# Kernel tuning notes

Measured on AMD Instinct MI355X. Metric: run time of the kernel, lower is better.

The kernel has to match this reference:

```python
import jax, jax.numpy as jnp
import numpy as np

N_NODES = 100000
N_EDGES = 1600000
IN_CH = 64
HEADS = 8
OUT_CH = 16
NEG_SLOPE = 0.2  # PyG GATConv default


def setup_inputs() -> dict:
    key = jax.random.key(0)
    ks = jax.random.split(key, 6)
    x = jax.random.normal(ks[0], (N_NODES, IN_CH), dtype=jnp.float32)
    edge_index = jax.random.randint(ks[1], (2, N_EDGES), 0, N_NODES, dtype=jnp.int32)
    # learned parameters (PyG GATConv: shared lin for src/dst, att vectors, bias for concat output)
    W = jax.random.normal(ks[2], (HEADS * OUT_CH, IN_CH), dtype=jnp.float32) / np.sqrt(IN_CH)
    att_src = jax.random.normal(ks[3], (HEADS, OUT_CH), dtype=jnp.float32) / np.sqrt(OUT_CH)
    att_dst = jax.random.normal(ks[4], (HEADS, OUT_CH), dtype=jnp.float32) / np.sqrt(OUT_CH)
    bias = jax.random.normal(ks[5], (HEADS * OUT_CH,), dtype=jnp.float32) * 0.01
    return {"x": x, "edge_index": edge_index, "W": W,
            "att_src": att_src, "att_dst": att_dst, "bias": bias}


def reference(x, edge_index, W, att_src, att_dst, bias):
    n = x.shape[0]
    # linear projection -> [N, H, C]
    h = (x @ W.T).reshape(n, HEADS, OUT_CH)
    # per-node halves of the attention logit
    a_src = jnp.einsum('nhc,hc->nh', h, att_src)  # [N, H]
    a_dst = jnp.einsum('nhc,hc->nh', h, att_dst)  # [N, H]
    # add self loops (PyG default add_self_loops=True)
    loops = jnp.arange(n, dtype=edge_index.dtype)
    src = jnp.concatenate([edge_index[0], loops])
    dst = jnp.concatenate([edge_index[1], loops])
    # edge attention: leaky_relu then segment-softmax over incoming edges of dst
    e = jax.nn.leaky_relu(a_src[src] + a_dst[dst], NEG_SLOPE)  # [E+N, H]
    e_max = jax.ops.segment_max(e, dst, num_segments=n)
    e = jnp.exp(e - e_max[dst])
    denom = jax.ops.segment_sum(e, dst, num_segments=n)
    alpha = e / (denom[dst] + 1e-16)  # [E+N, H]
    # weighted scatter-add aggregation
    msg = h[src] * alpha[:, :, None]  # [E+N, H, C]
    out = jax.ops.segment_sum(msg, dst, num_segments=n).reshape(n, HEADS * OUT_CH)
    out = out + bias
    # unlinear: act='relu', norm=None
    return jax.nn.relu(out)
```

## Files before the change

kernel.cpp:

```cpp
#include <hip/hip_runtime.h>

#define N_NODESC 100000
#define N_EDGESC 1600000
#define HCC 128
#define E_TOTC (N_EDGESC + N_NODESC)
#define SCAN_NB 391
#define PROJ_NB 782
#define POS_NB 6641
#define WU_NB 36

#define FLAG_AGG 0x40000000u
#define FLAG_PRE 0x80000000u
#define VAL_MASK 0x3fffffffu

__device__ __forceinline__ float lrelu(float v) { return fmaxf(v, 0.2f * v); }
__device__ __forceinline__ unsigned short f2bf(float f) {
    unsigned u = __float_as_uint(f);
    unsigned r = ((u >> 16) & 1u) + 0x7fffu;
    return (unsigned short)((u + r) >> 16);
}

__global__ void wu_pos_kernel(const float* __restrict__ W,
                              const float* __restrict__ att_src, const float* __restrict__ att_dst,
                              float* __restrict__ WT, float* __restrict__ us_g,
                              const int* __restrict__ ei, int* __restrict__ deg,
                              int* __restrict__ posb) {
    if (blockIdx.x < WU_NB) {
        int t = blockIdx.x * 256 + threadIdx.x;
        if (t < 8192) {
            int k = t >> 7, c = t & 127;
            WT[t] = W[c * 64 + k];
        } else if (t < 9216) {
            int o = t - 8192;
            int k = o >> 4, c = o & 15;
            const int h = (c < 8) ? c : c - 8;
            const float* av = (c < 8) ? att_src : att_dst;
            float s = 0.f;
#pragma unroll
            for (int j = 0; j < 16; ++j) s += av[h * 16 + j] * W[(h * 16 + j) * 64 + k];
            us_g[o] = s;
        }
        return;
    }
    int e = (blockIdx.x - WU_NB) * 256 + threadIdx.x;
    if (e >= E_TOTC) return;
    int d = (e < N_EDGESC) ? ei[N_EDGESC + e] : (e - N_EDGESC);
    posb[e] = atomicAdd(&deg[d], 1);
}

__launch_bounds__(256, 2)
__global__ void proj_kernel(const float* __restrict__ x, const float* __restrict__ WT,
                            const float* __restrict__ us_g,
                            unsigned short* __restrict__ h16,
                            float* __restrict__ a_src, float* __restrict__ a_dst) {
    __shared__ float xs[128][68];
    __shared__ float ws[64][132];
    __shared__ float us[64][16];
    const int t = threadIdx.x;
    const int row0 = blockIdx.x * 128;

    const float4* wt4 = (const float4*)WT;
#pragma unroll
    for (int j = 0; j < 8; ++j) {
        int q = t + 256 * j;
        int k = q >> 5, c4 = q & 31;
        *(float4*)&ws[k][c4 * 4] = wt4[q];
    }
    ((float4*)&us[0][0])[t] = ((const float4*)us_g)[t];

#pragma unroll
    for (int j = 0; j < 8; ++j) {
        int f = (t + 256 * j) * 4;
        int r = f >> 6, k = f & 63;
        int gr = row0 + r;
        if (gr >= N_NODESC) gr = N_NODESC - 1;
        float4 v = *(const float4*)&x[(size_t)gr * 64 + k];
        *(float4*)&xs[r][k] = v;
    }
    __syncthreads();

    const int rg = t & 15;
    const int cg = t >> 4;
    float acc[8][8], acca[8];
#pragma unroll
    for (int i = 0; i < 8; ++i) {
        acca[i] = 0.f;
#pragma unroll
        for (int j = 0; j < 8; ++j) acc[i][j] = 0.f;
    }

#pragma unroll 4
    for (int k = 0; k < 64; ++k) {
        float xv[8];
#pragma unroll
        for (int i = 0; i < 8; ++i) xv[i] = xs[rg + 16 * i][k];
        float4 w0 = *(const float4*)&ws[k][4 * cg];
        float4 w1 = *(const float4*)&ws[k][64 + 4 * cg];
        float uv = us[k][cg];
#pragma unroll
        for (int i = 0; i < 8; ++i) {
            acc[i][0] += xv[i] * w0.x; acc[i][1] += xv[i] * w0.y;
            acc[i][2] += xv[i] * w0.z; acc[i][3] += xv[i] * w0.w;
            acc[i][4] += xv[i] * w1.x; acc[i][5] += xv[i] * w1.y;
            acc[i][6] += xv[i] * w1.z; acc[i][7] += xv[i] * w1.w;
            acca[i]   += xv[i] * uv;
        }
    }

#pragma unroll
    for (int i = 0; i < 8; ++i) {
        int gr = row0 + rg + 16 * i;
        if (gr < N_NODESC) {
            ushort4 p0, p1;
            p0.x = f2bf(acc[i][0]); p0.y = f2bf(acc[i][1]); p0.z = f2bf(acc[i][2]); p0.w = f2bf(acc[i][3]);
            p1.x = f2bf(acc[i][4]); p1.y = f2bf(acc[i][5]); p1.z = f2bf(acc[i][6]); p1.w = f2bf(acc[i][7]);
            *(ushort4*)&h16[(size_t)gr * HCC + 4 * cg] = p0;
            *(ushort4*)&h16[(size_t)gr * HCC + 64 + 4 * cg] = p1;
            if (cg < 8) a_src[(size_t)gr * 8 + cg] = acca[i];
            else        a_dst[(size_t)gr * 8 + cg - 8] = acca[i];
        }
    }
}

__global__ void scan_kernel(const int* __restrict__ deg, unsigned* __restrict__ state,
                            int* __restrict__ rowptr) {
    __shared__ int lds[256];
    __shared__ int s_prefix;
    const int b = blockIdx.x, t = threadIdx.x;
    const int i = b * 256 + t;
    const int v = (i < N_NODESC) ? deg[i] : 0;
    lds[t] = v;
    __syncthreads();
    for (int off = 1; off < 256; off <<= 1) {
        int u = 0;
        if (t >= off) u = lds[t - off];
        __syncthreads();
        if (t >= off) lds[t] += u;
        __syncthreads();
    }
    const int incl = lds[t];
    const int total = lds[255];
    if (t == 0) {
        if (b == 0) {
            atomicExch(&state[0], FLAG_PRE | (unsigned)total);
            s_prefix = 0;
        } else {
            atomicExch(&state[b], FLAG_AGG | (unsigned)total);
            unsigned run = 0;
            int j = b - 1;
            while (true) {
                unsigned s = atomicAdd(&state[j], 0u);
                if (s & FLAG_PRE) { run += s & VAL_MASK; break; }
                if (s & FLAG_AGG) { run += s & VAL_MASK; --j; }
            }
            atomicExch(&state[b], FLAG_PRE | ((unsigned)total + run));
            s_prefix = (int)run;
        }
    }
    __syncthreads();
    const int excl = s_prefix + incl - v;
    if (i <= N_NODESC) rowptr[i] = excl;
}

__global__ void scatter_kernel(const int* __restrict__ ei, const int* __restrict__ rowptr,
                               const int* __restrict__ posb, int* __restrict__ colsrc) {
    int e = blockIdx.x * 256 + threadIdx.x;
    if (e >= E_TOTC) return;
    int s, d;
    if (e < N_EDGESC) { s = ei[e]; d = ei[N_EDGESC + e]; }
    else              { s = d = e - N_EDGESC; }
    colsrc[rowptr[d] + posb[e]] = s;
}

__launch_bounds__(256, 8)
__global__ void agg_csr_kernel(const int* __restrict__ rowptr, const int* __restrict__ colsrc,
                               const float* __restrict__ a_src, const float* __restrict__ a_dst,
                               const unsigned* __restrict__ h32,
                               const float* __restrict__ bias, float* __restrict__ out) {
    const int t = threadIdx.x;
    const int L = t & 63;
    const int n = blockIdx.x * 4 + (t >> 6);
    const int hd = L >> 3;
    const int eL = L & 7;

    const int beg = rowptr[n], end = rowptr[n + 1];
    const float ad = a_dst[n * 8 + hd];

    float den = 0.f;
    float acc[16];
#pragma unroll
    for (int j = 0; j < 16; ++j) acc[j] = 0.f;

    int p = beg + eL;
    bool v0 = p < end;
    bool v1 = p + 8 < end;
    int sA = v0 ? colsrc[p] : 0;
    int sB = v1 ? colsrc[p + 8] : 0;
    float avA = v0 ? a_src[sA * 8 + hd] : 0.f;

    while (v0) {
        const uint4* hp = (const uint4*)(h32 + (size_t)sA * 64 + hd * 8);
        const uint4 ha = hp[0];
        const uint4 hb = hp[1];
        const bool v2 = p + 16 < end;
        const int sC = v2 ? colsrc[p + 16] : 0;
        const float avB = v1 ? a_src[sB * 8 + hd] : 0.f;

        const float pr = __expf(lrelu(avA + ad));
        den += pr;
        acc[0]  = fmaf(pr, __uint_as_float(ha.x << 16),         acc[0]);
        acc[1]  = fmaf(pr, __uint_as_float(ha.x & 0xffff0000u), acc[1]);
        acc[2]  = fmaf(pr, __uint_as_float(ha.y << 16),         acc[2]);
        acc[3]  = fmaf(pr, __uint_as_float(ha.y & 0xffff0000u), acc[3]);
        acc[4]  = fmaf(pr, __uint_as_float(ha.z << 16),         acc[4]);
        acc[5]  = fmaf(pr, __uint_as_float(ha.z & 0xffff0000u), acc[5]);
        acc[6]  = fmaf(pr, __uint_as_float(ha.w << 16),         acc[6]);
        acc[7]  = fmaf(pr, __uint_as_float(ha.w & 0xffff0000u), acc[7]);
        acc[8]  = fmaf(pr, __uint_as_float(hb.x << 16),         acc[8]);
        acc[9]  = fmaf(pr, __uint_as_float(hb.x & 0xffff0000u), acc[9]);
        acc[10] = fmaf(pr, __uint_as_float(hb.y << 16),         acc[10]);
        acc[11] = fmaf(pr, __uint_as_float(hb.y & 0xffff0000u), acc[11]);
        acc[12] = fmaf(pr, __uint_as_float(hb.z << 16),         acc[12]);
        acc[13] = fmaf(pr, __uint_as_float(hb.z & 0xffff0000u), acc[13]);
        acc[14] = fmaf(pr, __uint_as_float(hb.w << 16),         acc[14]);
        acc[15] = fmaf(pr, __uint_as_float(hb.w & 0xffff0000u), acc[15]);

        p += 8;
        sA = sB; sB = sC; avA = avB;
        v0 = v1; v1 = v2;
    }

    den += __shfl_xor(den, 1); den += __shfl_xor(den, 2); den += __shfl_xor(den, 4);
#pragma unroll
    for (int j = 0; j < 16; ++j) {
        acc[j] += __shfl_xor(acc[j], 1);
        acc[j] += __shfl_xor(acc[j], 2);
        acc[j] += __shfl_xor(acc[j], 4);
    }
    const float inv = 1.f / (den + 1e-16f);
    float ox = acc[0], oy = acc[1];
#pragma unroll
    for (int j = 1; j < 8; ++j) {
        ox = (eL == j) ? acc[2 * j]     : ox;
        oy = (eL == j) ? acc[2 * j + 1] : oy;
    }
    const float2 b = ((const float2*)bias)[L];
    float2 o;
    o.x = fmaxf(ox * inv + b.x, 0.f);
    o.y = fmaxf(oy * inv + b.y, 0.f);
    ((float2*)out)[(size_t)n * 64 + L] = o;
}

extern "C" void kernel_launch(void* const* d_in, const int* in_sizes, int n_in,
                              void* d_out, int out_size, void* d_ws, size_t ws_size,
                              hipStream_t stream) {
    const float* x       = (const float*)d_in[0];
    const int*   ei      = (const int*)d_in[1];
    const float* W       = (const float*)d_in[2];
    const float* att_src = (const float*)d_in[3];
    const float* att_dst = (const float*)d_in[4];
    const float* bias    = (const float*)d_in[5];
    float* out = (float*)d_out;

    float* ws    = (float*)d_ws;
    unsigned short* h16 = (unsigned short*)ws;
    float* a_src = ws + 6400000;
    float* a_dst = a_src + 800000;
    float* WT    = a_dst + 800000;
    float* us_g  = WT + 8192;
    int* deg     = (int*)(us_g + 1024);
    unsigned* state = (unsigned*)(deg + 100000);
    int* rowptr  = (int*)(state + 392);
    int* posb    = rowptr + 100001;
    int* colsrc  = posb + 1700000;

    hipMemsetAsync(deg, 0, (100000 + 392) * sizeof(int), stream);

    wu_pos_kernel<<<WU_NB + POS_NB, 256, 0, stream>>>(W, att_src, att_dst, WT, us_g,
                                                      ei, deg, posb);
    proj_kernel<<<PROJ_NB, 256, 0, stream>>>(x, WT, us_g, h16, a_src, a_dst);
    scan_kernel<<<SCAN_NB, 256, 0, stream>>>(deg, state, rowptr);
    scatter_kernel<<<(E_TOTC + 255) / 256, 256, 0, stream>>>(ei, rowptr, posb, colsrc);
    agg_csr_kernel<<<N_NODESC / 4, 256, 0, stream>>>(rowptr, colsrc, a_src, a_dst,
                                                     (const unsigned*)h16, bias, out);
}
```

Measured before the change: 234.9 us.

## Store features in head-major planes and split aggregation per head

The projection now writes h, a_src and a_dst in head-major planes so each head's data is contiguous. Aggregation launches eight times as many blocks, one head per block, and each lane handles two channels for one edge slot. The aim is a smaller per-head working set that stays in cache during random neighbor gathers, plus fewer registers per thread. In exchange, each edge's colsrc and rowptr is read eight times, gathers shrink to 4 bytes, and seven of every eight lanes sit idle at write-out.

```diff
diff --git a/kernel.cpp b/kernel.cpp
--- a/kernel.cpp
+++ b/kernel.cpp
@@ -51,8 +51,8 @@
 __launch_bounds__(256, 2)
 __global__ void proj_kernel(const float* __restrict__ x, const float* __restrict__ WT,
                             const float* __restrict__ us_g,
-                            unsigned short* __restrict__ h16,
-                            float* __restrict__ a_src, float* __restrict__ a_dst) {
+                            unsigned short* __restrict__ hplane,
+                            float* __restrict__ a_src_p, float* __restrict__ a_dst_p) {
     __shared__ float xs[128][68];
     __shared__ float ws[64][132];
     __shared__ float us[64][16];
@@ -107,6 +107,8 @@
         }
     }
 
+    const int hA = cg >> 2, hB = 4 + (cg >> 2);
+    const int o4 = 4 * (cg & 3);
 #pragma unroll
     for (int i = 0; i < 8; ++i) {
         int gr = row0 + rg + 16 * i;
@@ -114,10 +116,10 @@
             ushort4 p0, p1;
             p0.x = f2bf(acc[i][0]); p0.y = f2bf(acc[i][1]); p0.z = f2bf(acc[i][2]); p0.w = f2bf(acc[i][3]);
             p1.x = f2bf(acc[i][4]); p1.y = f2bf(acc[i][5]); p1.z = f2bf(acc[i][6]); p1.w = f2bf(acc[i][7]);
-            *(ushort4*)&h16[(size_t)gr * HCC + 4 * cg] = p0;
-            *(ushort4*)&h16[(size_t)gr * HCC + 64 + 4 * cg] = p1;
-            if (cg < 8) a_src[(size_t)gr * 8 + cg] = acca[i];
-            else        a_dst[(size_t)gr * 8 + cg - 8] = acca[i];
+            *(ushort4*)&hplane[((size_t)hA * N_NODESC + gr) * 16 + o4] = p0;
+            *(ushort4*)&hplane[((size_t)hB * N_NODESC + gr) * 16 + o4] = p1;
+            if (cg < 8) a_src_p[(size_t)cg * N_NODESC + gr] = acca[i];
+            else        a_dst_p[(size_t)(cg - 8) * N_NODESC + gr] = acca[i];
         }
     }
 }
@@ -173,82 +175,59 @@
 }
 
 __launch_bounds__(256, 8)
-__global__ void agg_csr_kernel(const int* __restrict__ rowptr, const int* __restrict__ colsrc,
-                               const float* __restrict__ a_src, const float* __restrict__ a_dst,
-                               const unsigned* __restrict__ h32,
-                               const float* __restrict__ bias, float* __restrict__ out) {
+__global__ void agg_head_kernel(const int* __restrict__ rowptr, const int* __restrict__ colsrc,
+                                const float* __restrict__ a_src_p, const float* __restrict__ a_dst_p,
+                                const unsigned short* __restrict__ hplane,
+                                const float* __restrict__ bias, float* __restrict__ out) {
     const int t = threadIdx.x;
     const int L = t & 63;
-    const int n = blockIdx.x * 4 + (t >> 6);
-    const int hd = L >> 3;
-    const int eL = L & 7;
+    const int head = blockIdx.x & 7;
+    const int n = (blockIdx.x >> 3) * 4 + (t >> 6);
+    const int e = L & 7;
+    const int g = L >> 3;
 
     const int beg = rowptr[n], end = rowptr[n + 1];
-    const float ad = a_dst[n * 8 + hd];
-
-    float den = 0.f;
-    float acc[16];
-#pragma unroll
-    for (int j = 0; j < 16; ++j) acc[j] = 0.f;
-
-    int p = beg + eL;
+    const float ad = a_dst_p[(size_t)head * N_NODESC + n];
+    const unsigned short* hp_base = hplane + (size_t)head * N_NODESC * 16 + 2 * g;
+    const float* as_base = a_src_p + (size_t)head * N_NODESC;
+
+    float den = 0.f, acc0 = 0.f, acc1 = 0.f;
+
+    int p = beg + e;
     bool v0 = p < end;
     bool v1 = p + 8 < end;
     int sA = v0 ? colsrc[p] : 0;
     int sB = v1 ? colsrc[p + 8] : 0;
-    float avA = v0 ? a_src[sA * 8 + hd] : 0.f;
+    float avA = v0 ? as_base[sA] : 0.f;
 
     while (v0) {
-        const uint4* hp = (const uint4*)(h32 + (size_t)sA * 64 + hd * 8);
-        const uint4 ha = hp[0];
-        const uint4 hb = hp[1];
+        const unsigned hv = *(const unsigned*)(hp_base + (size_t)sA * 16);
         const bool v2 = p + 16 < end;
         const int sC = v2 ? colsrc[p + 16] : 0;
-        const float avB = v1 ? a_src[sB * 8 + hd] : 0.f;
+        const float avB = v1 ? as_base[sB] : 0.f;
 
         const float pr = __expf(lrelu(avA + ad));
         den += pr;
-        acc[0]  = fmaf(pr, __uint_as_float(ha.x << 16),         acc[0]);
-        acc[1]  = fmaf(pr, __uint_as_float(ha.x & 0xffff0000u), acc[1]);
-        acc[2]  = fmaf(pr, __uint_as_float(ha.y << 16),         acc[2]);
-        acc[3]  = fmaf(pr, __uint_as_float(ha.y & 0xffff0000u), acc[3]);
-        acc[4]  = fmaf(pr, __uint_as_float(ha.z << 16),         acc[4]);
-        acc[5]  = fmaf(pr, __uint_as_float(ha.z & 0xffff0000u), acc[5]);
-        acc[6]  = fmaf(pr, __uint_as_float(ha.w << 16),         acc[6]);
-        acc[7]  = fmaf(pr, __uint_as_float(ha.w & 0xffff0000u), acc[7]);
-        acc[8]  = fmaf(pr, __uint_as_float(hb.x << 16),         acc[8]);
-        acc[9]  = fmaf(pr, __uint_as_float(hb.x & 0xffff0000u), acc[9]);
-        acc[10] = fmaf(pr, __uint_as_float(hb.y << 16),         acc[10]);
-        acc[11] = fmaf(pr, __uint_as_float(hb.y & 0xffff0000u), acc[11]);
-        acc[12] = fmaf(pr, __uint_as_float(hb.z << 16),         acc[12]);
-        acc[13] = fmaf(pr, __uint_as_float(hb.z & 0xffff0000u), acc[13]);
-        acc[14] = fmaf(pr, __uint_as_float(hb.w << 16),         acc[14]);
-        acc[15] = fmaf(pr, __uint_as_float(hb.w & 0xffff0000u), acc[15]);
+        acc0 = fmaf(pr, __uint_as_float(hv << 16),         acc0);
+        acc1 = fmaf(pr, __uint_as_float(hv & 0xffff0000u), acc1);
 
         p += 8;
         sA = sB; sB = sC; avA = avB;
         v0 = v1; v1 = v2;
     }
 
-    den += __shfl_xor(den, 1); den += __shfl_xor(den, 2); den += __shfl_xor(den, 4);
-#pragma unroll
-    for (int j = 0; j < 16; ++j) {
-        acc[j] += __shfl_xor(acc[j], 1);
-        acc[j] += __shfl_xor(acc[j], 2);
-        acc[j] += __shfl_xor(acc[j], 4);
-    }
-    const float inv = 1.f / (den + 1e-16f);
-    float ox = acc[0], oy = acc[1];
-#pragma unroll
-    for (int j = 1; j < 8; ++j) {
-        ox = (eL == j) ? acc[2 * j]     : ox;
-        oy = (eL == j) ? acc[2 * j + 1] : oy;
-    }
-    const float2 b = ((const float2*)bias)[L];
-    float2 o;
-    o.x = fmaxf(ox * inv + b.x, 0.f);
-    o.y = fmaxf(oy * inv + b.y, 0.f);
-    ((float2*)out)[(size_t)n * 64 + L] = o;
+    den  += __shfl_xor(den, 1);  den  += __shfl_xor(den, 2);  den  += __shfl_xor(den, 4);
+    acc0 += __shfl_xor(acc0, 1); acc0 += __shfl_xor(acc0, 2); acc0 += __shfl_xor(acc0, 4);
+    acc1 += __shfl_xor(acc1, 1); acc1 += __shfl_xor(acc1, 2); acc1 += __shfl_xor(acc1, 4);
+
+    if (e == 0) {
+        const float inv = 1.f / (den + 1e-16f);
+        const float2 b = *(const float2*)&bias[head * 16 + 2 * g];
+        float2 o;
+        o.x = fmaxf(acc0 * inv + b.x, 0.f);
+        o.y = fmaxf(acc1 * inv + b.y, 0.f);
+        *(float2*)&out[(size_t)n * HCC + head * 16 + 2 * g] = o;
+    }
 }
 
 extern "C" void kernel_launch(void* const* d_in, const int* in_sizes, int n_in,
@@ -263,10 +242,10 @@
     float* out = (float*)d_out;
 
     float* ws    = (float*)d_ws;
-    unsigned short* h16 = (unsigned short*)ws;
-    float* a_src = ws + 6400000;
-    float* a_dst = a_src + 800000;
-    float* WT    = a_dst + 800000;
+    unsigned short* hplane = (unsigned short*)ws;
+    float* a_src_p = ws + 6400000;
+    float* a_dst_p = a_src_p + 800000;
+    float* WT    = a_dst_p + 800000;
     float* us_g  = WT + 8192;
     int* deg     = (int*)(us_g + 1024);
     unsigned* state = (unsigned*)(deg + 100000);
@@ -278,9 +257,9 @@
 
     wu_pos_kernel<<<WU_NB + POS_NB, 256, 0, stream>>>(W, att_src, att_dst, WT, us_g,
                                                       ei, deg, posb);
-    proj_kernel<<<PROJ_NB, 256, 0, stream>>>(x, WT, us_g, h16, a_src, a_dst);
+    proj_kernel<<<PROJ_NB, 256, 0, stream>>>(x, WT, us_g, hplane, a_src_p, a_dst_p);
     scan_kernel<<<SCAN_NB, 256, 0, stream>>>(deg, state, rowptr);
     scatter_kernel<<<(E_TOTC + 255) / 256, 256, 0, stream>>>(ei, rowptr, posb, colsrc);
-    agg_csr_kernel<<<N_NODESC / 4, 256, 0, stream>>>(rowptr, colsrc, a_src, a_dst,
-                                                     (const unsigned*)h16, bias, out);
-}
+    agg_head_kernel<<<(N_NODESC / 4) * 8, 256, 0, stream>>>(rowptr, colsrc, a_src_p, a_dst_p,
+                                                            hplane, bias, out);
+}
```

Measured after the change: 415.7 us. 77.0% more time.

## Fuse projection, degree count, scan and scatter into one persistent kernel with grid barriers

Applied to the files above, without the earlier changes.

Merges the weight-transpose, degree/position atomics, projection GEMM, decoupled-lookback scan and CSR scatter into a single persistent kernel of 448 blocks. Some blocks run the projection tiles while the others do the degree atomics at the same time, and software grid barriers separate the scan and scatter phases. Edge work now moves four edges per thread using int4 loads. This is meant to remove three kernel launches and to overlap the compute-bound projection with the atomic-bound counting. The risks are deadlock if not all 448 blocks are co-resident, and extra cost from spin-waiting on the barriers.

```diff
diff --git a/kernel.cpp b/kernel.cpp
--- a/kernel.cpp
+++ b/kernel.cpp
@@ -4,10 +4,11 @@
 #define N_EDGESC 1600000
 #define HCC 128
 #define E_TOTC (N_EDGESC + N_NODESC)
+#define E_QUADS (E_TOTC / 4)
 #define SCAN_NB 391
 #define PROJ_NB 782
-#define POS_NB 6641
-#define WU_NB 36
+#define BUILD_NB 448
+#define PROJ_ROLE 320
 
 #define FLAG_AGG 0x40000000u
 #define FLAG_PRE 0x80000000u
@@ -20,156 +21,186 @@
     return (unsigned short)((u + r) >> 16);
 }
 
-__global__ void wu_pos_kernel(const float* __restrict__ W,
-                              const float* __restrict__ att_src, const float* __restrict__ att_dst,
-                              float* __restrict__ WT, float* __restrict__ us_g,
-                              const int* __restrict__ ei, int* __restrict__ deg,
-                              int* __restrict__ posb) {
-    if (blockIdx.x < WU_NB) {
-        int t = blockIdx.x * 256 + threadIdx.x;
-        if (t < 8192) {
-            int k = t >> 7, c = t & 127;
-            WT[t] = W[c * 64 + k];
-        } else if (t < 9216) {
-            int o = t - 8192;
-            int k = o >> 4, c = o & 15;
-            const int h = (c < 8) ? c : c - 8;
-            const float* av = (c < 8) ? att_src : att_dst;
-            float s = 0.f;
-#pragma unroll
-            for (int j = 0; j < 16; ++j) s += av[h * 16 + j] * W[(h * 16 + j) * 64 + k];
-            us_g[o] = s;
-        }
-        return;
-    }
-    int e = (blockIdx.x - WU_NB) * 256 + threadIdx.x;
-    if (e >= E_TOTC) return;
-    int d = (e < N_EDGESC) ? ei[N_EDGESC + e] : (e - N_EDGESC);
-    posb[e] = atomicAdd(&deg[d], 1);
+__device__ __forceinline__ void gridbar(int* c) {
+    __syncthreads();
+    if (threadIdx.x == 0) {
+        __threadfence();
+        atomicAdd(c, 1);
+        while (atomicAdd(c, 0) < BUILD_NB) { }
+    }
+    __syncthreads();
 }
 
 __launch_bounds__(256, 2)
-__global__ void proj_kernel(const float* __restrict__ x, const float* __restrict__ WT,
-                            const float* __restrict__ us_g,
-                            unsigned short* __restrict__ h16,
-                            float* __restrict__ a_src, float* __restrict__ a_dst) {
+__global__ void build_kernel(const float* __restrict__ x, const float* __restrict__ W,
+                             const float* __restrict__ att_src, const float* __restrict__ att_dst,
+                             const int* __restrict__ ei,
+                             unsigned short* __restrict__ h16,
+                             float* __restrict__ a_src, float* __restrict__ a_dst,
+                             int* __restrict__ deg, int* __restrict__ posb,
+                             unsigned* __restrict__ state, int* __restrict__ rowptr,
+                             int* __restrict__ colsrc, int* __restrict__ bar) {
     __shared__ float xs[128][68];
     __shared__ float ws[64][132];
     __shared__ float us[64][16];
-    const int t = threadIdx.x;
-    const int row0 = blockIdx.x * 128;
-
-    const float4* wt4 = (const float4*)WT;
-#pragma unroll
-    for (int j = 0; j < 8; ++j) {
-        int q = t + 256 * j;
-        int k = q >> 5, c4 = q & 31;
-        *(float4*)&ws[k][c4 * 4] = wt4[q];
-    }
-    ((float4*)&us[0][0])[t] = ((const float4*)us_g)[t];
-
-#pragma unroll
-    for (int j = 0; j < 8; ++j) {
-        int f = (t + 256 * j) * 4;
-        int r = f >> 6, k = f & 63;
-        int gr = row0 + r;
-        if (gr >= N_NODESC) gr = N_NODESC - 1;
-        float4 v = *(const float4*)&x[(size_t)gr * 64 + k];
-        *(float4*)&xs[r][k] = v;
-    }
-    __syncthreads();
-
-    const int rg = t & 15;
-    const int cg = t >> 4;
-    float acc[8][8], acca[8];
-#pragma unroll
-    for (int i = 0; i < 8; ++i) {
-        acca[i] = 0.f;
-#pragma unroll
-        for (int j = 0; j < 8; ++j) acc[i][j] = 0.f;
-    }
-
-#pragma unroll 4
-    for (int k = 0; k < 64; ++k) {
-        float xv[8];
-#pragma unroll
-        for (int i = 0; i < 8; ++i) xv[i] = xs[rg + 16 * i][k];
-        float4 w0 = *(const float4*)&ws[k][4 * cg];
-        float4 w1 = *(const float4*)&ws[k][64 + 4 * cg];
-        float uv = us[k][cg];
-#pragma unroll
-        for (int i = 0; i < 8; ++i) {
-            acc[i][0] += xv[i] * w0.x; acc[i][1] += xv[i] * w0.y;
-            acc[i][2] += xv[i] * w0.z; acc[i][3] += xv[i] * w0.w;
-            acc[i][4] += xv[i] * w1.x; acc[i][5] += xv[i] * w1.y;
-            acc[i][6] += xv[i] * w1.z; acc[i][7] += xv[i] * w1.w;
-            acca[i]   += xv[i] * uv;
-        }
-    }
-
-#pragma unroll
-    for (int i = 0; i < 8; ++i) {
-        int gr = row0 + rg + 16 * i;
-        if (gr < N_NODESC) {
-            ushort4 p0, p1;
-            p0.x = f2bf(acc[i][0]); p0.y = f2bf(acc[i][1]); p0.z = f2bf(acc[i][2]); p0.w = f2bf(acc[i][3]);
-            p1.x = f2bf(acc[i][4]); p1.y = f2bf(acc[i][5]); p1.z = f2bf(acc[i][6]); p1.w = f2bf(acc[i][7]);
-            *(ushort4*)&h16[(size_t)gr * HCC + 4 * cg] = p0;
-            *(ushort4*)&h16[(size_t)gr * HCC + 64 + 4 * cg] = p1;
-            if (cg < 8) a_src[(size_t)gr * 8 + cg] = acca[i];
-            else        a_dst[(size_t)gr * 8 + cg - 8] = acca[i];
-        }
-    }
-}
-
-__global__ void scan_kernel(const int* __restrict__ deg, unsigned* __restrict__ state,
-                            int* __restrict__ rowptr) {
-    __shared__ int lds[256];
+    __shared__ int slds[256];
     __shared__ int s_prefix;
     const int b = blockIdx.x, t = threadIdx.x;
-    const int i = b * 256 + t;
-    const int v = (i < N_NODESC) ? deg[i] : 0;
-    lds[t] = v;
-    __syncthreads();
-    for (int off = 1; off < 256; off <<= 1) {
-        int u = 0;
-        if (t >= off) u = lds[t - off];
+
+    if (b < PROJ_ROLE) {
+        const float4* W4 = (const float4*)W;
+#pragma unroll
+        for (int j = 0; j < 8; ++j) {
+            int q = t + 256 * j;
+            float4 v = W4[q];
+            int c = q >> 4, k0 = (q & 15) * 4;
+            ws[k0 + 0][c] = v.x; ws[k0 + 1][c] = v.y;
+            ws[k0 + 2][c] = v.z; ws[k0 + 3][c] = v.w;
+        }
+#pragma unroll
+        for (int j = 0; j < 4; ++j) {
+            int o = t + 256 * j;
+            int k = o >> 4, c = o & 15;
+            const int h = c & 7;
+            const float* av = (c < 8) ? att_src : att_dst;
+            float s = 0.f;
+#pragma unroll
+            for (int jj = 0; jj < 16; ++jj) s += av[h * 16 + jj] * W[(h * 16 + jj) * 64 + k];
+            us[k][c] = s;
+        }
+
+        for (int tile = b; tile < PROJ_NB; tile += PROJ_ROLE) {
+            const int row0 = tile * 128;
+            __syncthreads();
+#pragma unroll
+            for (int j = 0; j < 8; ++j) {
+                int f = (t + 256 * j) * 4;
+                int r = f >> 6, k = f & 63;
+                int gr = row0 + r;
+                if (gr >= N_NODESC) gr = N_NODESC - 1;
+                float4 v = *(const float4*)&x[(size_t)gr * 64 + k];
+                *(float4*)&xs[r][k] = v;
+            }
+            __syncthreads();
+
+            const int rg = t & 15;
+            const int cg = t >> 4;
+            float acc[8][8], acca[8];
+#pragma unroll
+            for (int i = 0; i < 8; ++i) {
+                acca[i] = 0.f;
+#pragma unroll
+                for (int j = 0; j < 8; ++j) acc[i][j] = 0.f;
+            }
+#pragma unroll 4
+            for (int k = 0; k < 64; ++k) {
+                float xv[8];
+#pragma unroll
+                for (int i = 0; i < 8; ++i) xv[i] = xs[rg + 16 * i][k];
+                float4 w0 = *(const float4*)&ws[k][4 * cg];
+                float4 w1 = *(const float4*)&ws[k][64 + 4 * cg];
+                float uv = us[k][cg];
+#pragma unroll
+                for (int i = 0; i < 8; ++i) {
+                    acc[i][0] += xv[i] * w0.x; acc[i][1] += xv[i] * w0.y;
+                    acc[i][2] += xv[i] * w0.z; acc[i][3] += xv[i] * w0.w;
+                    acc[i][4] += xv[i] * w1.x; acc[i][5] += xv[i] * w1.y;
+                    acc[i][6] += xv[i] * w1.z; acc[i][7] += xv[i] * w1.w;
+                    acca[i]   += xv[i] * uv;
+                }
+            }
+#pragma unroll
+            for (int i = 0; i < 8; ++i) {
+                int gr = row0 + rg + 16 * i;
+                if (gr < N_NODESC) {
+                    ushort4 p0, p1;
+                    p0.x = f2bf(acc[i][0]); p0.y = f2bf(acc[i][1]); p0.z = f2bf(acc[i][2]); p0.w = f2bf(acc[i][3]);
+                    p1.x = f2bf(acc[i][4]); p1.y = f2bf(acc[i][5]); p1.z = f2bf(acc[i][6]); p1.w = f2bf(acc[i][7]);
+                    *(ushort4*)&h16[(size_t)gr * HCC + 4 * cg] = p0;
+                    *(ushort4*)&h16[(size_t)gr * HCC + 64 + 4 * cg] = p1;
+                    if (cg < 8) a_src[(size_t)gr * 8 + cg] = acca[i];
+                    else        a_dst[(size_t)gr * 8 + cg - 8] = acca[i];
+                }
+            }
+        }
+    } else {
+        const int qid = (b - PROJ_ROLE) * 256 + t;
+        const int qstride = (BUILD_NB - PROJ_ROLE) * 256;
+        for (int q = qid; q < E_QUADS; q += qstride) {
+            const int e0 = q * 4;
+            int d[4], p[4];
+            if (e0 < N_EDGESC) {
+                int4 dd = *(const int4*)&ei[N_EDGESC + e0];
+                d[0] = dd.x; d[1] = dd.y; d[2] = dd.z; d[3] = dd.w;
+            } else {
+#pragma unroll
+                for (int j = 0; j < 4; ++j) d[j] = e0 + j - N_EDGESC;
+            }
+#pragma unroll
+            for (int j = 0; j < 4; ++j) p[j] = atomicAdd(&deg[d[j]], 1);
+            *(int4*)&posb[e0] = make_int4(p[0], p[1], p[2], p[3]);
+        }
+    }
+
+    gridbar(&bar[0]);
+
+    if (b < SCAN_NB) {
+        const int i = b * 256 + t;
+        const int v = (i < N_NODESC) ? deg[i] : 0;
+        slds[t] = v;
         __syncthreads();
-        if (t >= off) lds[t] += u;
+        for (int off = 1; off < 256; off <<= 1) {
+            int u = 0;
+            if (t >= off) u = slds[t - off];
+            __syncthreads();
+            if (t >= off) slds[t] += u;
+            __syncthreads();
+        }
+        const int incl = slds[t];
+        const int total = slds[255];
+        if (t == 0) {
+            if (b == 0) {
+                atomicExch(&state[0], FLAG_PRE | (unsigned)total);
+                s_prefix = 0;
+            } else {
+                atomicExch(&state[b], FLAG_AGG | (unsigned)total);
+                unsigned run = 0;
+                int j = b - 1;
+                while (true) {
+                    unsigned s = atomicAdd(&state[j], 0u);
+                    if (s & FLAG_PRE) { run += s & VAL_MASK; break; }
+                    if (s & FLAG_AGG) { run += s & VAL_MASK; --j; }
+                }
+                atomicExch(&state[b], FLAG_PRE | ((unsigned)total + run));
+                s_prefix = (int)run;
+            }
+        }
         __syncthreads();
-    }
-    const int incl = lds[t];
-    const int total = lds[255];
-    if (t == 0) {
-        if (b == 0) {
-            atomicExch(&state[0], FLAG_PRE | (unsigned)total);
-            s_prefix = 0;
+        const int excl = s_prefix + incl - v;
+        if (i <= N_NODESC) rowptr[i] = excl;
+    }
+
+    gridbar(&bar[1]);
+
+    for (int q = b * 256 + t; q < E_QUADS; q += BUILD_NB * 256) {
+        const int e0 = q * 4;
+        int4 pp = *(const int4*)&posb[e0];
+        int s[4], d[4], p[4] = { pp.x, pp.y, pp.z, pp.w };
+        if (e0 < N_EDGESC) {
+            int4 ss = *(const int4*)&ei[e0];
+            int4 dd = *(const int4*)&ei[N_EDGESC + e0];
+            s[0] = ss.x; s[1] = ss.y; s[2] = ss.z; s[3] = ss.w;
+            d[0] = dd.x; d[1] = dd.y; d[2] = dd.z; d[3] = dd.w;
         } else {
-            atomicExch(&state[b], FLAG_AGG | (unsigned)total);
-            unsigned run = 0;
-            int j = b - 1;
-            while (true) {
-                unsigned s = atomicAdd(&state[j], 0u);
-                if (s & FLAG_PRE) { run += s & VAL_MASK; break; }
-                if (s & FLAG_AGG) { run += s & VAL_MASK; --j; }
-            }
-            atomicExch(&state[b], FLAG_PRE | ((unsigned)total + run));
-            s_prefix = (int)run;
-        }
-    }
-    __syncthreads();
-    const int excl = s_prefix + incl - v;
-    if (i <= N_NODESC) rowptr[i] = excl;
-}
-
-__global__ void scatter_kernel(const int* __restrict__ ei, const int* __restrict__ rowptr,
-                               const int* __restrict__ posb, int* __restrict__ colsrc) {
-    int e = blockIdx.x * 256 + threadIdx.x;
-    if (e >= E_TOTC) return;
-    int s, d;
-    if (e < N_EDGESC) { s = ei[e]; d = ei[N_EDGESC + e]; }
-    else              { s = d = e - N_EDGESC; }
-    colsrc[rowptr[d] + posb[e]] = s;
+#pragma unroll
+            for (int j = 0; j < 4; ++j) { s[j] = d[j] = e0 + j - N_EDGESC; }
+        }
+        int r[4];
+#pragma unroll
+        for (int j = 0; j < 4; ++j) r[j] = rowptr[d[j]];
+#pragma unroll
+        for (int j = 0; j < 4; ++j) colsrc[r[j] + p[j]] = s[j];
+    }
 }
 
 __launch_bounds__(256, 8)
@@ -266,21 +297,18 @@
     unsigned short* h16 = (unsigned short*)ws;
     float* a_src = ws + 6400000;
     float* a_dst = a_src + 800000;
-    float* WT    = a_dst + 800000;
-    float* us_g  = WT + 8192;
-    int* deg     = (int*)(us_g + 1024);
+    int* deg     = (int*)(a_dst + 800000);
     unsigned* state = (unsigned*)(deg + 100000);
-    int* rowptr  = (int*)(state + 392);
+    int* bar     = (int*)(state + 392);
+    int* rowptr  = bar + 8;
     int* posb    = rowptr + 100001;
     int* colsrc  = posb + 1700000;
 
-    hipMemsetAsync(deg, 0, (100000 + 392) * sizeof(int), stream);
-
-    wu_pos_kernel<<<WU_NB + POS_NB, 256, 0, stream>>>(W, att_src, att_dst, WT, us_g,
-                                                      ei, deg, posb);
-    proj_kernel<<<PROJ_NB, 256, 0, stream>>>(x, WT, us_g, h16, a_src, a_dst);
-    scan_kernel<<<SCAN_NB, 256, 0, stream>>>(deg, state, rowptr);
-    scatter_kernel<<<(E_TOTC + 255) / 256, 256, 0, stream>>>(ei, rowptr, posb, colsrc);
+    hipMemsetAsync(deg, 0, (100000 + 392 + 8) * sizeof(int), stream);
+
+    build_kernel<<<BUILD_NB, 256, 0, stream>>>(x, W, att_src, att_dst, ei,
+                                               h16, a_src, a_dst,
+                                               deg, posb, state, rowptr, colsrc, bar);
     agg_csr_kernel<<<N_NODESC / 4, 256, 0, stream>>>(rowptr, colsrc, a_src, a_dst,
                                                      (const unsigned*)h16, bias, out);
 }
```

After: 285.8 us. +21.7%, slower.
